# Performance work log

Hardware: AMD Instinct MI355X
Metric: run time of the kernel (lower is better)

The kernel has to match this reference:

```python
import jax, jax.numpy as jnp
import numpy as np


def setup_inputs() -> dict:
    key = jax.random.key(0)
    k1, k2, k3, k4 = jax.random.split(key, 4)
    B, T, D, H = 64, 256, 2048, 2048
    scale_w = 1.0 / np.sqrt(D)
    scale_h = 1.0 / np.sqrt(H)
    return {
        "x": jax.random.normal(k1, (B, T, D), dtype=jnp.float32),
        "W": jax.random.normal(k2, (D, H), dtype=jnp.float32) * scale_w,
        "Wh": jax.random.normal(k3, (H, H), dtype=jnp.float32) * scale_h,
        "b": jax.random.normal(k4, (H,), dtype=jnp.float32) * 0.01,
    }


def reference(x, W, Wh, b):
    """Elman RNN: h_t = tanh(x_t @ W + h_{t-1} @ Wh + b), h_0 = 0.
    return_sequences=False and activation=identity, so output is the final state.
    (The original computes step 0 with a zero state then loops t=1..T-1, which
    is exactly a scan over all T steps starting from h=0.)"""
    B, T, D = x.shape
    H = Wh.shape[0]
    # Precompute the input projection for all timesteps in one big GEMM.
    xw = jnp.einsum('btd,dh->tbh', x, W) + b  # [T, B, H]

    def step(h, xw_t):
        h = jnp.tanh(xw_t + h @ Wh)
        return h, None

    h0 = jnp.zeros((B, H), dtype=x.dtype)
    h_last, _ = jax.lax.scan(step, h0, xw)
    return h_last  # [B, H]
```

## Files before the change

### kernel.cpp

```cpp
#include <hip/hip_runtime.h>
#include <hip/hip_bf16.h>
#include <hip/hip_fp16.h>

typedef _Float16 f16;
typedef _Float16 f16x8 __attribute__((ext_vector_type(8)));
typedef float f32x4 __attribute__((ext_vector_type(4)));
typedef unsigned int u32;
typedef unsigned long long u64;

#define HB 2048
#define DD 2048
#define TT 256
#define BB 64

typedef const __attribute__((address_space(1))) u32 gu32;
typedef __attribute__((address_space(3))) u32 lu32;

__device__ __forceinline__ void gl_lds16(const void* g, void* l) {
    __builtin_amdgcn_global_load_lds((gu32*)g, (lu32*)l, 16, 0, 0);
}

#define LOADM_SC0(dst, ar)                                                    \
    asm volatile("global_load_dwordx4 %0, %8, off sc0\n\t"                    \
                 "global_load_dwordx4 %1, %8, off offset:64 sc0\n\t"          \
                 "global_load_dwordx4 %2, %8, off offset:128 sc0\n\t"         \
                 "global_load_dwordx4 %3, %8, off offset:192 sc0\n\t"         \
                 "global_load_dwordx4 %4, %8, off offset:256 sc0\n\t"         \
                 "global_load_dwordx4 %5, %8, off offset:320 sc0\n\t"         \
                 "global_load_dwordx4 %6, %8, off offset:384 sc0\n\t"         \
                 "global_load_dwordx4 %7, %8, off offset:448 sc0"             \
                 : "=&v"(dst[0]), "=&v"(dst[1]), "=&v"(dst[2]), "=&v"(dst[3]),\
                   "=&v"(dst[4]), "=&v"(dst[5]), "=&v"(dst[6]), "=&v"(dst[7]) \
                 : "v"(ar)                                                    \
                 : "memory")

#define VMCNT0 asm volatile("s_waitcnt vmcnt(0)" ::: "memory")
#define VMCNT4 asm volatile("s_waitcnt vmcnt(4)" ::: "memory")

__device__ __forceinline__ u32 ld_flag_sc0(const u32* p) {
    u32 v;
    asm volatile("global_load_dword %0, %1, off sc0\n\ts_waitcnt vmcnt(0)"
                 : "=v"(v) : "v"(p) : "memory");
    return v;
}
__device__ __forceinline__ u32 ld_flag_sc1(const u32* p) {
    u32 v;
    asm volatile("global_load_dword %0, %1, off sc1\n\ts_waitcnt vmcnt(0)"
                 : "=v"(v) : "v"(p) : "memory");
    return v;
}

__global__ __launch_bounds__(256) void k_transpose_cvt(const float* __restrict__ src,
                                                       f16* __restrict__ dst) {
    __shared__ f16 tile[64][65];
    int bx = blockIdx.x * 64;
    int by = blockIdx.y * 64;
    int tx = threadIdx.x & 63;
    int ty = threadIdx.x >> 6;
#pragma unroll
    for (int r = ty; r < 64; r += 4)
        tile[r][tx] = (f16)src[(size_t)(by + r) * HB + bx + tx];
    __syncthreads();
#pragma unroll
    for (int r = ty; r < 64; r += 4)
        dst[(size_t)(bx + r) * HB + by + tx] = tile[tx][r];
}

__global__ __launch_bounds__(256) void k_cvt_x(const float* __restrict__ x,
                                               f16* __restrict__ a16) {
    int r = blockIdx.x;
    int d = threadIdx.x * 8;
    const float* src = x + ((size_t)(r & 63) * TT + (r >> 6)) * DD + d;
    float4 v0 = *(const float4*)src;
    float4 v1 = *(const float4*)(src + 4);
    f16x8 o = {(f16)v0.x, (f16)v0.y, (f16)v0.z, (f16)v0.w,
               (f16)v1.x, (f16)v1.y, (f16)v1.z, (f16)v1.w};
    *(f16x8*)(a16 + (size_t)r * DD + d) = o;
}

__global__ __launch_bounds__(256) void k_gemm_xw_lds(const f16* __restrict__ a16,
                                                     const f16* __restrict__ W16T,
                                                     const float* __restrict__ bias,
                                                     f16* __restrict__ xw16) {
    __shared__ f16 As[128 * 32];
    __shared__ f16 Bs[128 * 32];
    int tid = threadIdx.x;
    int lane = tid & 63, w = tid >> 6;
    int wr = w >> 1, wc = w & 1;
    int lr = lane & 15, kg = lane >> 4;
    int rowBase = blockIdx.y * 128;
    int colBase = blockIdx.x * 128;

    f32x4 acc[4][4] = {};

    int r0 = tid >> 2, c0 = ((tid & 3) ^ ((r0 >> 1) & 3)) * 8;
    int u1 = tid + 256;
    int r1 = u1 >> 2, c1 = ((u1 & 3) ^ ((r1 >> 1) & 3)) * 8;
    const f16* gA0 = a16 + (size_t)(rowBase + r0) * DD + c0;
    const f16* gA1 = a16 + (size_t)(rowBase + r1) * DD + c1;
    const f16* gB0 = W16T + (size_t)(colBase + r0) * DD + c0;
    const f16* gB1 = W16T + (size_t)(colBase + r1) * DD + c1;
    f16* lA0 = As + (size_t)(w * 64) * 8;
    f16* lA1 = As + (size_t)(256 + w * 64) * 8;
    f16* lB0 = Bs + (size_t)(w * 64) * 8;
    f16* lB1 = Bs + (size_t)(256 + w * 64) * 8;

    for (int kk = 0; kk < DD; kk += 32) {
        gl_lds16(gA0 + kk, lA0);
        gl_lds16(gA1 + kk, lA1);
        gl_lds16(gB0 + kk, lB0);
        gl_lds16(gB1 + kk, lB1);
        __syncthreads();

        f16x8 af[4], bf[4];
#pragma unroll
        for (int mi = 0; mi < 4; ++mi) {
            int row = wr * 64 + mi * 16 + lr;
            af[mi] = *(const f16x8*)(As + row * 32 + (kg ^ ((row >> 1) & 3)) * 8);
        }
#pragma unroll
        for (int ni = 0; ni < 4; ++ni) {
            int rowb = wc * 64 + ni * 16 + lr;
            bf[ni] = *(const f16x8*)(Bs + rowb * 32 + (kg ^ ((rowb >> 1) & 3)) * 8);
        }
#pragma unroll
        for (int mi = 0; mi < 4; ++mi)
#pragma unroll
            for (int ni = 0; ni < 4; ++ni)
                acc[mi][ni] = __builtin_amdgcn_mfma_f32_16x16x32_f16(af[mi], bf[ni],
                                                                     acc[mi][ni], 0, 0, 0);
        __syncthreads();
    }

#pragma unroll
    for (int mi = 0; mi < 4; ++mi)
#pragma unroll
        for (int ni = 0; ni < 4; ++ni) {
            int col = colBase + wc * 64 + ni * 16 + lr;
            float bv = bias[col];
#pragma unroll
            for (int j = 0; j < 4; ++j) {
                int row = rowBase + wr * 64 + mi * 16 + kg * 4 + j;
                xw16[(size_t)row * HB + col] = (f16)(acc[mi][ni][j] + bv);
            }
        }
}

__global__ __launch_bounds__(256) void k_gemm_xw_direct(const float* __restrict__ x,
                                                        const f16* __restrict__ W16T,
                                                        const float* __restrict__ bias,
                                                        f16* __restrict__ xw16) {
    int lane = threadIdx.x & 63;
    int w = threadIdx.x >> 6;
    int wr = w >> 1, wc = w & 1;
    int rowBase = blockIdx.y * 64 + wr * 32;
    int colBase = blockIdx.x * 64 + wc * 32;
    int lr = lane & 15;
    int kg = lane >> 4;

    f32x4 acc[2][2] = {};

    int r0 = rowBase + lr;
    int r1 = rowBase + 16 + lr;
    const float* xrow0 = x + ((size_t)(r0 & 63) * TT + (r0 >> 6)) * DD;
    const float* xrow1 = x + ((size_t)(r1 & 63) * TT + (r1 >> 6)) * DD;
    const f16* wrow0 = W16T + (size_t)(colBase + lr) * DD;
    const f16* wrow1 = W16T + (size_t)(colBase + 16 + lr) * DD;

    for (int kk = 0; kk < DD; kk += 32) {
        int k = kk + kg * 8;
        const float4* pa0 = reinterpret_cast<const float4*>(xrow0 + k);
        const float4* pa1 = reinterpret_cast<const float4*>(xrow1 + k);
        float4 a0l = pa0[0], a0h = pa0[1];
        float4 a1l = pa1[0], a1h = pa1[1];
        f16x8 a0 = {(f16)a0l.x, (f16)a0l.y, (f16)a0l.z, (f16)a0l.w,
                    (f16)a0h.x, (f16)a0h.y, (f16)a0h.z, (f16)a0h.w};
        f16x8 a1 = {(f16)a1l.x, (f16)a1l.y, (f16)a1l.z, (f16)a1l.w,
                    (f16)a1h.x, (f16)a1h.y, (f16)a1h.z, (f16)a1h.w};
        f16x8 b0 = *reinterpret_cast<const f16x8*>(wrow0 + k);
        f16x8 b1 = *reinterpret_cast<const f16x8*>(wrow1 + k);
        acc[0][0] = __builtin_amdgcn_mfma_f32_16x16x32_f16(a0, b0, acc[0][0], 0, 0, 0);
        acc[0][1] = __builtin_amdgcn_mfma_f32_16x16x32_f16(a0, b1, acc[0][1], 0, 0, 0);
        acc[1][0] = __builtin_amdgcn_mfma_f32_16x16x32_f16(a1, b0, acc[1][0], 0, 0, 0);
        acc[1][1] = __builtin_amdgcn_mfma_f32_16x16x32_f16(a1, b1, acc[1][1], 0, 0, 0);
    }

#pragma unroll
    for (int mi = 0; mi < 2; ++mi)
#pragma unroll
        for (int ni = 0; ni < 2; ++ni) {
            int col = colBase + ni * 16 + lr;
            float bv = bias[col];
#pragma unroll
            for (int j = 0; j < 4; ++j) {
                int row = rowBase + mi * 16 + kg * 4 + j;
                xw16[(size_t)row * HB + col] = (f16)(acc[mi][ni][j] + bv);
            }
        }
}

__global__ __launch_bounds__(128) void k_rnn_step(const f16* __restrict__ hin,
                                                  const f16* __restrict__ WhT,
                                                  const f16* __restrict__ xw_t,
                                                  f16* __restrict__ hout,
                                                  float* __restrict__ dout, int last,
                                                  int first) {
    int lane = threadIdx.x & 63;
    int w = threadIdx.x >> 6;
    int m0 = blockIdx.y * 32 + w * 16;
    int n0 = blockIdx.x * 16;
    int lr = lane & 15;
    int kg = lane >> 4;

    f32x4 acc = {};
    if (!first) {
        const f16* arow = hin + (size_t)(m0 + lr) * HB;
        const f16* brow = WhT + (size_t)(n0 + lr) * HB;
#pragma unroll 4
        for (int kk = 0; kk < HB; kk += 32) {
            int k = kk + kg * 8;
            f16x8 a = *reinterpret_cast<const f16x8*>(arow + k);
            f16x8 b = *reinterpret_cast<const f16x8*>(brow + k);
            acc = __builtin_amdgcn_mfma_f32_16x16x32_f16(a, b, acc, 0, 0, 0);
        }
    }

#pragma unroll
    for (int j = 0; j < 4; ++j) {
        int row = m0 + kg * 4 + j;
        int col = n0 + lr;
        float pre = acc[j] + (float)xw_t[(size_t)row * HB + col];
        float h = tanhf(pre);
        hout[(size_t)row * HB + col] = (f16)h;
        if (last) dout[(size_t)row * HB + col] = h;
    }
}

__global__ __launch_bounds__(512, 2) void k_rnn_persist(const f16* __restrict__ Wh16T,
                                                        const f16* __restrict__ xw16,
                                                        f16* __restrict__ hseq,
                                                        float* __restrict__ dout,
                                                        u32* __restrict__ bar) {
    __shared__ float red[2][8][8][68];
    __shared__ u32 ready_s;
    volatile u32* ready = &ready_s;
    int tid = threadIdx.x;
    int lane = tid & 63, w = tid >> 6;
    int lr = lane & 15, kg = lane >> 4;
    int g = blockIdx.x & 7;
    int j = blockIdx.x >> 3;
    int row0 = g * 8;
    int n0 = j * 64;

    if (tid == 0) *ready = 0;

    f16x8 bfrag[4][8];
#pragma unroll
    for (int n = 0; n < 4; ++n) {
        const f16* brow = Wh16T + (size_t)(n0 + n * 16 + lr) * DD + w * 256 + kg * 8;
#pragma unroll
        for (int s = 0; s < 8; ++s) bfrag[n][s] = *(const f16x8*)(brow + s * 32);
    }

    int f_row = tid >> 4;
    int f_c = (tid & 15) * 4;

    const u32* myflag =
        bar + (size_t)(((((u32)(lane >> 1) << 3) | g) << 1) | (lane & 1)) * 16;
    u32* ourflag = bar + (size_t)(((u32)blockIdx.x << 1) | (w & 1)) * 16;

    __syncthreads();

    u64 xwv_next = 0;
    if (tid < 128)
        xwv_next = *(const u64*)(xw16 + ((size_t)0 * BB + row0 + f_row) * HB + n0 + f_c);

    for (int t = 0; t < TT; ++t) {
        u64 xwv = xwv_next;

        f32x4 acc[4] = {};
        if (t > 0) {
            if (w == 7) {
                u32 tgt = (u32)t;
                u32 v = ld_flag_sc0(myflag);
                int tries = 0;
                while (!__all(v >= tgt)) {
                    __builtin_amdgcn_s_sleep(1);
                    v = (++tries < 8) ? ld_flag_sc0(myflag) : ld_flag_sc1(myflag);
                }
                if (lane == 0) *ready = (u32)t;
            } else {
                while (*ready < (u32)t) {  }
            }
            __builtin_amdgcn_sched_barrier(0);

            if (tid < 128 && t + 1 < TT)
                xwv_next = *(const u64*)(xw16 +
                                         ((size_t)(t + 1) * BB + row0 + f_row) * HB +
                                         n0 + f_c);

            const f16* abase = hseq + ((size_t)(t - 1) * BB + row0 + (lr & 7)) * HB +
                               w * 256 + kg * 8;
            f16x8 hv[8];
            LOADM_SC0(hv, abase);
            VMCNT4;
            __builtin_amdgcn_sched_barrier(0);
            if (lr >= 8) {
#pragma unroll
                for (int s = 0; s < 4; ++s) hv[s] = (f16x8)(f16)0;
            }
#pragma unroll
            for (int s = 0; s < 4; ++s)
#pragma unroll
                for (int n = 0; n < 4; ++n)
                    acc[n] = __builtin_amdgcn_mfma_f32_16x16x32_f16(hv[s], bfrag[n][s],
                                                                    acc[n], 0, 0, 0);
            VMCNT0;
            __builtin_amdgcn_sched_barrier(0);
            if (lr >= 8) {
#pragma unroll
                for (int s = 4; s < 8; ++s) hv[s] = (f16x8)(f16)0;
            }
#pragma unroll
            for (int s = 4; s < 8; ++s)
#pragma unroll
                for (int n = 0; n < 4; ++n)
                    acc[n] = __builtin_amdgcn_mfma_f32_16x16x32_f16(hv[s], bfrag[n][s],
                                                                    acc[n], 0, 0, 0);
        } else {
            if (tid < 128)
                xwv_next = *(const u64*)(xw16 + ((size_t)1 * BB + row0 + f_row) * HB +
                                         n0 + f_c);
        }

        if (kg < 2) {
#pragma unroll
            for (int n = 0; n < 4; ++n)
#pragma unroll
                for (int jj = 0; jj < 4; ++jj)
                    red[t & 1][w][kg * 4 + jj][n * 16 + lr] = acc[n][jj];
        }
        __syncthreads();

        if (tid < 128) {
            float4 sum = {0.f, 0.f, 0.f, 0.f};
#pragma unroll
            for (int ww = 0; ww < 8; ++ww) {
                float4 v = *(const float4*)&red[t & 1][ww][f_row][f_c];
                sum.x += v.x; sum.y += v.y; sum.z += v.z; sum.w += v.w;
            }
            union { u64 q; f16 h[4]; } xwu;
            xwu.q = xwv;
            float h0 = tanhf(sum.x + (float)xwu.h[0]);
            float h1 = tanhf(sum.y + (float)xwu.h[1]);
            float h2 = tanhf(sum.z + (float)xwu.h[2]);
            float h3 = tanhf(sum.w + (float)xwu.h[3]);

            if (t == TT - 1) {
                float4 o = {h0, h1, h2, h3};
                *(float4*)(dout + (size_t)(row0 + f_row) * HB + n0 + f_c) = o;
            } else {
                union { u64 q; f16 h[4]; } ho;
                ho.h[0] = (f16)h0; ho.h[1] = (f16)h1;
                ho.h[2] = (f16)h2; ho.h[3] = (f16)h3;
                u64* dst = (u64*)(hseq + ((size_t)t * BB + row0 + f_row) * HB + n0 + f_c);
                *(volatile u64*)dst = ho.q;
                VMCNT0;
                if ((tid & 63) == 0)
                    *(volatile u32*)ourflag = (u32)(t + 1);
                __hip_atomic_store(dst, ho.q, __ATOMIC_RELAXED,
                                   __HIP_MEMORY_SCOPE_AGENT);
                VMCNT0;
                if ((tid & 63) == 0)
                    __hip_atomic_store(ourflag, (u32)(t + 1), __ATOMIC_RELAXED,
                                       __HIP_MEMORY_SCOPE_AGENT);
            }
        }
    }
}

extern "C" void kernel_launch(void* const* d_in, const int* in_sizes, int n_in,
                              void* d_out, int out_size, void* d_ws, size_t ws_size,
                              hipStream_t stream) {
    const float* x = (const float*)d_in[0];
    const float* W = (const float*)d_in[1];
    const float* Wh = (const float*)d_in[2];
    const float* bias = (const float*)d_in[3];
    float* dout = (float*)d_out;

    char* ws = (char*)d_ws;
    const size_t SZ_WT = (size_t)HB * DD * 2;
    const size_t SZ_H = (size_t)BB * HB * 2;
    const size_t SZ_XW = (size_t)TT * BB * HB * 2;
    const size_t OFF_W = 0;
    const size_t OFF_WH = OFF_W + SZ_WT;
    const size_t OFF_H01 = OFF_WH + SZ_WT;
    const size_t OFF_BAR = OFF_H01 + 2 * SZ_H;
    const size_t OFF_XW = OFF_BAR + 65536;
    const size_t OFF_HSEQ = OFF_XW + SZ_XW;
    const size_t NEED_FULL = OFF_HSEQ + SZ_XW;

    f16* W16T = (f16*)(ws + OFF_W);
    f16* Wh16T = (f16*)(ws + OFF_WH);
    f16* h0 = (f16*)(ws + OFF_H01);
    f16* h1 = (f16*)(ws + OFF_H01 + SZ_H);
    u32* bar = (u32*)(ws + OFF_BAR);
    f16* xw16 = (f16*)(ws + OFF_XW);
    f16* hseq = (f16*)(ws + OFF_HSEQ);

    dim3 tgrid(32, 32);
    k_transpose_cvt<<<tgrid, 256, 0, stream>>>(W, W16T);
    k_transpose_cvt<<<tgrid, 256, 0, stream>>>(Wh, Wh16T);

    if (ws_size >= NEED_FULL) {
        f16* x16 = hseq;
        k_cvt_x<<<TT * BB, 256, 0, stream>>>(x, x16);
        k_gemm_xw_lds<<<dim3(HB / 128, TT * BB / 128), 256, 0, stream>>>(x16, W16T, bias, xw16);
        hipMemsetAsync(bar, 0, 65536, stream);
        k_rnn_persist<<<256, 512, 0, stream>>>(Wh16T, xw16, hseq, dout, bar);
    } else {
        k_gemm_xw_direct<<<dim3(HB / 64, TT * BB / 64), 256, 0, stream>>>(x, W16T, bias, xw16);
        f16* hb[2] = {h0, h1};
        for (int t = 0; t < TT; ++t) {
            const f16* xwt = xw16 + (size_t)t * BB * HB;
            k_rnn_step<<<dim3(128, 2), 128, 0, stream>>>(hb[t & 1], Wh16T, xwt,
                                                         hb[(t + 1) & 1], dout,
                                                         t == TT - 1, t == 0);
        }
    }
}
```

Baseline: 1.473 ms.

## Assign persistent RNN block roles by XCD to keep row groups on one die

Instead of deriving the row group and column tile from blockIdx, each block reads its XCD id from a hardware register and atomically claims a slot in the group matching its XCD. All blocks of a row group then tend to sit on the same die, so the per-step flag barrier and the h exchange stay inside one L2. This adds an atomic claim at startup and relies on the claim counters in the barrier buffer being zeroed before every launch.

```diff
diff --git a/kernel.cpp b/kernel.cpp
--- a/kernel.cpp
+++ b/kernel.cpp
@@ -243,17 +243,37 @@
                                                         u32* __restrict__ bar) {
     __shared__ float red[2][8][8][68];
     __shared__ u32 ready_s;
+    __shared__ u32 role_s;
     volatile u32* ready = &ready_s;
     int tid = threadIdx.x;
     int lane = tid & 63, w = tid >> 6;
     int lr = lane & 15, kg = lane >> 4;
-    int g = blockIdx.x & 7;
-    int j = blockIdx.x >> 3;
+
+    u32* claim = bar + 16000;
+    if (tid == 0) {
+        *ready = 0;
+        u32 xcd;
+        asm volatile("s_getreg_b32 %0, hwreg(20, 0, 32)" : "=s"(xcd));
+        xcd &= 7;
+        u32 role = 0;
+        for (int a = 0; a < 8; ++a) {
+            u32 gg = (xcd + (u32)a) & 7;
+            u32 n = __hip_atomic_fetch_add(&claim[gg], 1u, __ATOMIC_RELAXED,
+                                           __HIP_MEMORY_SCOPE_AGENT);
+            if (n < 32u) {
+                role = (n << 3) | gg;
+                break;
+            }
+        }
+        role_s = role;
+    }
+    __syncthreads();
+    u32 vbid = role_s;
+    int g = (int)(vbid & 7);
+    int j = (int)(vbid >> 3);
     int row0 = g * 8;
     int n0 = j * 64;
 
-    if (tid == 0) *ready = 0;
-
     f16x8 bfrag[4][8];
 #pragma unroll
     for (int n = 0; n < 4; ++n) {
@@ -266,8 +286,8 @@
     int f_c = (tid & 15) * 4;
 
     const u32* myflag =
-        bar + (size_t)(((((u32)(lane >> 1) << 3) | g) << 1) | (lane & 1)) * 16;
-    u32* ourflag = bar + (size_t)(((u32)blockIdx.x << 1) | (w & 1)) * 16;
+        bar + (size_t)(((((u32)(lane >> 1) << 3) | (u32)g) << 1) | (lane & 1)) * 16;
+    u32* ourflag = bar + (size_t)((vbid << 1) | (u32)(w & 1)) * 16;
 
     __syncthreads();
 
```

Measured after the change: 1.466 ms. No clear change (-0.5%).
